# Kernel tuning notes

Hardware: AMD Instinct MI355X
Metric: run time of the kernel (lower is better)

The kernel has to match this reference:

```python
import jax, jax.numpy as jnp
import numpy as np

N = 100000
E = 1600000
IN_C, HID_C, OUT_C = 128, 128, 47


def setup_inputs() -> dict:
    key = jax.random.key(0)
    ks = jax.random.split(key, 10)
    x = jax.random.normal(ks[0], (N, IN_C), dtype=jnp.float32)
    edge_index = jax.random.randint(ks[1], (2, E), 0, N, dtype=jnp.int64)
    edge_attr = jax.random.normal(ks[2], (E, 8), dtype=jnp.float32)
    # GCNConv weights (glorot-like scale) and biases
    W1 = jax.random.normal(ks[3], (IN_C, HID_C), dtype=jnp.float32) / np.sqrt(IN_C)
    b1 = jnp.zeros((HID_C,), dtype=jnp.float32)
    W2 = jax.random.normal(ks[4], (HID_C, HID_C), dtype=jnp.float32) / np.sqrt(HID_C)
    b2 = jnp.zeros((HID_C,), dtype=jnp.float32)
    W3 = jax.random.normal(ks[5], (HID_C, OUT_C), dtype=jnp.float32) / np.sqrt(HID_C)
    b3 = jnp.zeros((OUT_C,), dtype=jnp.float32)
    return {"x": x, "edge_index": edge_index, "edge_attr": edge_attr,
            "W1": W1, "b1": b1, "W2": W2, "b2": b2, "W3": W3, "b3": b3}


def _gcn_norm(edge_index, num_nodes):
    # GCNConv default: add self-loops, symmetric normalization D^-1/2 (A+I) D^-1/2
    row, col = edge_index[0], edge_index[1]
    deg = jax.ops.segment_sum(jnp.ones((edge_index.shape[1],), jnp.float32), row,
                              num_segments=num_nodes) + 1.0  # +1 for self-loop
    dis = jax.lax.rsqrt(deg)  # deg >= 1, always finite
    edge_norm = dis[row] * dis[col]   # [E]
    self_norm = dis * dis             # [N], self-loop weight
    return edge_norm, self_norm


def _gcn_conv(h, W, b, row, col, edge_norm, self_norm, num_nodes):
    h = h @ W                                  # linear transform first (PyG order)
    msg = edge_norm[:, None] * h[col]          # [E, C] gathered, normalized messages
    agg = jax.ops.segment_sum(msg, row, num_segments=num_nodes)
    return agg + self_norm[:, None] * h + b    # self-loop contribution + bias


def reference(x, edge_index, edge_attr, W1, b1, W2, b2, W3, b3):
    # edge_attr is accepted but unused, matching the original forward.
    row, col = edge_index[0], edge_index[1]
    edge_norm, self_norm = _gcn_norm(edge_index, N)
    # layer 1 + relu (dropout is identity in eval mode)
    h = _gcn_conv(x, W1, b1, row, col, edge_norm, self_norm, N)
    h = jax.nn.relu(h)
    # layer 2 + relu
    h = _gcn_conv(h, W2, b2, row, col, edge_norm, self_norm, N)
    h = jax.nn.relu(h)
    # final layer, no activation
    return _gcn_conv(h, W3, b3, row, col, edge_norm, self_norm, N)
```

## Files before the change

### kernel.cpp

```cpp
#include <hip/hip_runtime.h>
#include <hip/hip_fp16.h>
#include <cstdint>
#include <cstddef>

#define N_NODES 100000
#define N_EDGES 1600000
#define BSHIFT 9
#define BSIZE (1 << BSHIFT)
#define NB ((N_NODES + BSIZE - 1) >> BSHIFT)
#define PTILE 4096

typedef _Float16 half8 __attribute__((ext_vector_type(8)));
typedef float floatx4 __attribute__((ext_vector_type(4)));
typedef int v4i __attribute__((ext_vector_type(4)));

__device__ float llvm_amdgcn_raw_buffer_load_fp32(v4i srsrc, int voffset,
                                                  int soffset, int aux)
    __asm("llvm.amdgcn.raw.buffer.load.f32");

static __device__ __forceinline__ v4i make_srsrc(const void* p) {
    unsigned long long a = (unsigned long long)p;
    v4i r;
    r[0] = (int)(unsigned)(a & 0xFFFFFFFFull);
    r[1] = (int)(unsigned)((a >> 32) & 0xFFFFull);
    r[2] = -1;
    r[3] = 0x00020000;
    return r;
}

static __device__ __forceinline__ __half2 f_as_h2(float f) {
    union { float f; __half2 h; } u; u.f = f; return u.h;
}

static __device__ __forceinline__ int edge_row(const void* ei, int i64, int e) {
    return i64 ? (int)((const long long*)ei)[e] : ((const int*)ei)[e];
}
static __device__ __forceinline__ int edge_col(const void* ei, int i64, int e) {
    return i64 ? (int)((const long long*)ei)[N_EDGES + e] : ((const int*)ei)[N_EDGES + e];
}

__global__ void __launch_bounds__(1024)
detect_i64(const int* __restrict__ w, int* __restrict__ flag,
           int* __restrict__ bsize) {
    __shared__ int red[1024];
    const int tid = threadIdx.x;
    if (tid < NB + 1) bsize[tid] = 0;
    int acc = 0;
    for (int j = tid; j < 2048; j += 1024) {
        int k = j * 781;
        acc |= w[2 * k + 1];
    }
    red[tid] = acc;
    __syncthreads();
    for (int off = 512; off > 0; off >>= 1) {
        if (tid < off) red[tid] |= red[tid + off];
        __syncthreads();
    }
    if (tid == 0) *flag = (red[0] == 0) ? 1 : 0;
}

__global__ void __launch_bounds__(256)
hist_buckets(const void* __restrict__ ei, const int* __restrict__ flag,
             int* __restrict__ bsize) {
    __shared__ int h[256];
    const int tid = threadIdx.x;
    const int tbase = blockIdx.x * PTILE;
    const int f = *flag;
    h[tid] = 0;
    __syncthreads();
    #pragma unroll
    for (int j = 0; j < PTILE / 256; ++j) {
        int idx = tbase + tid + j * 256;
        if (idx < N_EDGES) {
            int r = edge_row(ei, f, idx);
            atomicAdd(&h[r >> BSHIFT], 1);
        }
    }
    __syncthreads();
    if (tid < NB && h[tid] > 0) atomicAdd(&bsize[tid], h[tid]);
}

__global__ void scan_buckets(const int* __restrict__ bsize, int* __restrict__ bbase,
                             int* __restrict__ bcur) {
    __shared__ int sd[256];
    int t = threadIdx.x;
    int v = (t < NB) ? bsize[t] : 0;
    sd[t] = v;
    __syncthreads();
    for (int off = 1; off < 256; off <<= 1) {
        int add = (t >= off) ? sd[t - off] : 0;
        __syncthreads();
        sd[t] += add;
        __syncthreads();
    }
    if (t < NB) {
        bbase[t] = sd[t] - v;
        bcur[t] = sd[t] - v;
    }
    if (t == 255) bbase[NB] = sd[255];
}

__global__ void __launch_bounds__(256)
partition_edges(const void* __restrict__ ei, const int* __restrict__ flag,
                int* __restrict__ bcur, int* __restrict__ bktRow,
                int* __restrict__ bktCol) {
    __shared__ int rows[PTILE];
    __shared__ int cols[PTILE];
    __shared__ int h[256], sc[256], exs[256], base_s[256], p[256];

    const int tid = threadIdx.x;
    const int tbase = blockIdx.x * PTILE;
    const int tot = min(PTILE, N_EDGES - tbase);
    const int f = *flag;

    h[tid] = 0;
    p[tid] = 0;
    __syncthreads();

    #pragma unroll
    for (int j = 0; j < PTILE / 256; ++j) {
        int idx = tbase + tid + j * 256;
        if (idx < N_EDGES) {
            int r = edge_row(ei, f, idx);
            atomicAdd(&h[r >> BSHIFT], 1);
        }
    }
    __syncthreads();

    sc[tid] = h[tid];
    __syncthreads();
    for (int off = 1; off < 256; off <<= 1) {
        int v = (tid >= off) ? sc[tid - off] : 0;
        __syncthreads();
        sc[tid] += v;
        __syncthreads();
    }
    exs[tid] = sc[tid] - h[tid];
    if (tid < NB && h[tid] > 0) base_s[tid] = atomicAdd(&bcur[tid], h[tid]);
    __syncthreads();

    #pragma unroll
    for (int j = 0; j < PTILE / 256; ++j) {
        int idx = tbase + tid + j * 256;
        if (idx < N_EDGES) {
            int r = edge_row(ei, f, idx);
            int c = edge_col(ei, f, idx);
            int b = r >> BSHIFT;
            int lp = atomicAdd(&p[b], 1);
            int slot = exs[b] + lp;
            rows[slot] = r;
            cols[slot] = c;
        }
    }
    __syncthreads();

    for (int slot = tid; slot < tot; slot += 256) {
        int r = rows[slot];
        int b = r >> BSHIFT;
        int addr = base_s[b] + (slot - exs[b]);
        bktRow[addr] = r;
        bktCol[addr] = cols[slot];
    }
}

__global__ void __launch_bounds__(512)
bucket_stats(const int* __restrict__ bktRow, const int* __restrict__ bbase,
             int* __restrict__ deg, int* __restrict__ rowst,
             float* __restrict__ dis) {
    __shared__ int cnt[512];
    __shared__ int sd[512];
    const int b = blockIdx.x;
    const int t = threadIdx.x;
    const int start = bbase[b], end = bbase[b + 1];
    cnt[t] = 0;
    __syncthreads();
    for (int i = start + t; i < end; i += 512)
        atomicAdd(&cnt[bktRow[i] - (b << BSHIFT)], 1);
    __syncthreads();
    int v = cnt[t];
    sd[t] = v;
    __syncthreads();
    for (int off = 1; off < 512; off <<= 1) {
        int add = (t >= off) ? sd[t - off] : 0;
        __syncthreads();
        sd[t] += add;
        __syncthreads();
    }
    int node = (b << BSHIFT) + t;
    if (node < N_NODES) {
        deg[node] = v;
        rowst[node] = start + sd[t] - v;
        dis[node] = rsqrtf((float)v + 1.0f);
    }
}

__global__ void __launch_bounds__(512)
scatter_bucket(const int* __restrict__ bktRow, const int* __restrict__ bktCol,
               const int* __restrict__ bbase, const int* __restrict__ rowst,
               const float* __restrict__ dis, int2* __restrict__ csr_cn) {
    __shared__ int cur[512];
    __shared__ float dl[512];
    const int b = blockIdx.x;
    const int t = threadIdx.x;
    const int start = bbase[b], end = bbase[b + 1];
    int node = (b << BSHIFT) + t;
    cur[t] = (node < N_NODES) ? rowst[node] : 0;
    dl[t]  = (node < N_NODES) ? dis[node] : 0.f;
    __syncthreads();
    for (int i = start + t; i < end; i += 512) {
        int r = bktRow[i];
        int c = bktCol[i];
        int lr = r - (b << BSHIFT);
        int pos = atomicAdd(&cur[lr], 1);
        float nrm = dl[lr] * dis[c];
        csr_cn[pos] = make_int2(c, __float_as_int(nrm));
    }
}

template<typename TIn, int NT>
__global__ void __launch_bounds__(256)
gemm_mfma(const TIn* __restrict__ in, const float* __restrict__ W,
          __half* __restrict__ out, int Mfull, int ostride) {
    constexpr int NCOL = NT * 16;
    __shared__ _Float16 Wt[NCOL * 128];

    const int tid = threadIdx.x;
    for (int chunkIdx = tid; chunkIdx < NCOL * 16; chunkIdx += 256) {
        int n = chunkIdx % NCOL;
        int c = chunkIdx / NCOL;
        half8 v;
        #pragma unroll
        for (int i = 0; i < 8; ++i) {
            int k = c * 8 + i;
            v[i] = (n < Mfull) ? (_Float16)W[k * Mfull + n] : (_Float16)0.f;
        }
        *(half8*)&Wt[n * 128 + (c ^ (n & 7)) * 8] = v;
    }
    __syncthreads();

    const int wave = tid >> 6, lane = tid & 63;
    const int quad = lane >> 4, m = lane & 15;
    const int rowbase = blockIdx.x * 64 + wave * 16;
    const int arow_i = rowbase + m;
    const bool avalid = arow_i < N_NODES;
    const TIn* arow = in + (size_t)(avalid ? arow_i : 0) * 128;

    half8 a[4];
    #pragma unroll
    for (int kt = 0; kt < 4; ++kt) {
        if constexpr (sizeof(TIn) == 4) {
            const float4* ptr = (const float4*)((const float*)arow + kt * 32 + quad * 8);
            float4 f0 = ptr[0];
            float4 f1 = ptr[1];
            a[kt][0] = (_Float16)f0.x; a[kt][1] = (_Float16)f0.y;
            a[kt][2] = (_Float16)f0.z; a[kt][3] = (_Float16)f0.w;
            a[kt][4] = (_Float16)f1.x; a[kt][5] = (_Float16)f1.y;
            a[kt][6] = (_Float16)f1.z; a[kt][7] = (_Float16)f1.w;
        } else {
            a[kt] = *(const half8*)((const _Float16*)arow + kt * 32 + quad * 8);
        }
    }

    floatx4 acc[NT];
    #pragma unroll
    for (int ct = 0; ct < NT; ++ct) acc[ct] = (floatx4){0.f, 0.f, 0.f, 0.f};

    #pragma unroll
    for (int ct = 0; ct < NT; ++ct) {
        #pragma unroll
        for (int kt = 0; kt < 4; ++kt) {
            int n = ct * 16 + m;
            half8 bfrag = *(const half8*)&Wt[n * 128 + ((kt * 4 + quad) ^ (m & 7)) * 8];
            acc[ct] = __builtin_amdgcn_mfma_f32_16x16x32_f16(a[kt], bfrag, acc[ct], 0, 0, 0);
        }
    }

    const int rs0 = rowbase + quad * 4;
    #pragma unroll
    for (int ct = 0; ct < NT; ++ct) {
        int col = ct * 16 + m;
        if (col >= Mfull) continue;
        #pragma unroll
        for (int r = 0; r < 4; ++r) {
            int rs = rs0 + r;
            if (rs < N_NODES)
                out[(size_t)rs * ostride + col] = __float2half(acc[ct][r]);
        }
    }
}

#define AGG_DEPTH 6
#define AGG_BLOCKS 2048

__global__ void __launch_bounds__(256)
agg_c128(const __half* __restrict__ t, const int* __restrict__ rowst,
         const int* __restrict__ deg, const int2* __restrict__ cn,
         const float* __restrict__ dis, const float* __restrict__ bias,
         __half* __restrict__ out, int relu) {
    const int gwave = blockIdx.x * (blockDim.x >> 6) + (threadIdx.x >> 6);
    const int nw = gridDim.x * (blockDim.x >> 6);
    const int lane = threadIdx.x & 63;
    const float2 bv = ((const float2*)bias)[lane];
    const v4i trsrc = make_srsrc(t);
    const int voff_lane = lane << 2;

    for (int w = gwave; w < N_NODES; w += nw) {
        int s = rowst[w], d = deg[w];
        float di = dis[w];
        float sn = di * di;
        float2 tv = __half22float2(((const __half2*)(t + (size_t)w * 128))[lane]);
        float ax = fmaf(sn, tv.x, bv.x);
        float ay = fmaf(sn, tv.y, bv.y);
        int e = s + d;
        int j = s;
        if (j + AGG_DEPTH <= e) {
            int2 c[AGG_DEPTH];
            #pragma unroll
            for (int q = 0; q < AGG_DEPTH; ++q) c[q] = cn[j + q];
            j += AGG_DEPTH;
            while (j + AGG_DEPTH <= e) {
                int2 n[AGG_DEPTH];
                #pragma unroll
                for (int q = 0; q < AGG_DEPTH; ++q) n[q] = cn[j + q];
                __half2 v[AGG_DEPTH];
                #pragma unroll
                for (int q = 0; q < AGG_DEPTH; ++q)
                    v[q] = f_as_h2(llvm_amdgcn_raw_buffer_load_fp32(
                        trsrc, (c[q].x << 8) | voff_lane, 0, 1));
                #pragma unroll
                for (int q = 0; q < AGG_DEPTH; ++q) {
                    float2 fv = __half22float2(v[q]);
                    float nw2 = __int_as_float(c[q].y);
                    ax = fmaf(nw2, fv.x, ax);
                    ay = fmaf(nw2, fv.y, ay);
                }
                #pragma unroll
                for (int q = 0; q < AGG_DEPTH; ++q) c[q] = n[q];
                j += AGG_DEPTH;
            }
            #pragma unroll
            for (int q = 0; q < AGG_DEPTH; ++q) {
                __half2 vv = f_as_h2(llvm_amdgcn_raw_buffer_load_fp32(
                    trsrc, (c[q].x << 8) | voff_lane, 0, 1));
                float2 fv = __half22float2(vv);
                float nw2 = __int_as_float(c[q].y);
                ax = fmaf(nw2, fv.x, ax);
                ay = fmaf(nw2, fv.y, ay);
            }
        }
        for (; j < e; ++j) {
            int2 c = cn[j];
            __half2 vv = f_as_h2(llvm_amdgcn_raw_buffer_load_fp32(
                trsrc, (c.x << 8) | voff_lane, 0, 1));
            float2 fv = __half22float2(vv);
            float nw2 = __int_as_float(c.y);
            ax = fmaf(nw2, fv.x, ax);
            ay = fmaf(nw2, fv.y, ay);
        }
        if (relu) { ax = fmaxf(ax, 0.f); ay = fmaxf(ay, 0.f); }
        ((__half2*)(out + (size_t)w * 128))[lane] = __float22half2_rn(make_float2(ax, ay));
    }
}

#define C47_DEPTH 4

__global__ void __launch_bounds__(256)
agg_c47(const __half* __restrict__ t, const int* __restrict__ rowst,
        const int* __restrict__ deg, const int2* __restrict__ cn,
        const float* __restrict__ dis, const float* __restrict__ bias,
        float* __restrict__ out) {
    const int gwave = blockIdx.x * (blockDim.x >> 6) + (threadIdx.x >> 6);
    const int nw = gridDim.x * (blockDim.x >> 6);
    const int lane = threadIdx.x & 63;
    const int hw = lane >> 5;
    const int l2 = lane & 31;
    const int ch0 = l2 * 2, ch1 = ch0 + 1;
    const float b0 = (ch0 < 47) ? bias[ch0] : 0.f;
    const float b1 = (ch1 < 47) ? bias[ch1] : 0.f;

    for (int w = gwave; w < N_NODES; w += nw) {
        int s = rowst[w], d = deg[w];
        float di = dis[w];
        float sn = di * di;
        float2 tv = __half22float2(((const __half2*)(t + (size_t)w * 64))[l2]);
        float ax = (hw == 0) ? sn * tv.x : 0.f;
        float ay = (hw == 0) ? sn * tv.y : 0.f;
        int e = s + d;
        int j = s + hw;
        if (j + 2 * C47_DEPTH <= e + 1) {
            int2 c[C47_DEPTH];
            #pragma unroll
            for (int q = 0; q < C47_DEPTH; ++q) c[q] = cn[j + 2 * q];
            j += 2 * C47_DEPTH;
            while (j + 2 * C47_DEPTH <= e + 1) {
                int2 n[C47_DEPTH];
                #pragma unroll
                for (int q = 0; q < C47_DEPTH; ++q) n[q] = cn[j + 2 * q];
                __half2 v[C47_DEPTH];
                #pragma unroll
                for (int q = 0; q < C47_DEPTH; ++q)
                    v[q] = ((const __half2*)(t + (size_t)c[q].x * 64))[l2];
                #pragma unroll
                for (int q = 0; q < C47_DEPTH; ++q) {
                    float2 fv = __half22float2(v[q]);
                    float nw2 = __int_as_float(c[q].y);
                    ax = fmaf(nw2, fv.x, ax);
                    ay = fmaf(nw2, fv.y, ay);
                }
                #pragma unroll
                for (int q = 0; q < C47_DEPTH; ++q) c[q] = n[q];
                j += 2 * C47_DEPTH;
            }
            #pragma unroll
            for (int q = 0; q < C47_DEPTH; ++q) {
                __half2 vv = ((const __half2*)(t + (size_t)c[q].x * 64))[l2];
                float2 fv = __half22float2(vv);
                float nw2 = __int_as_float(c[q].y);
                ax = fmaf(nw2, fv.x, ax);
                ay = fmaf(nw2, fv.y, ay);
            }
        }
        for (; j < e; j += 2) {
            int2 c = cn[j];
            float2 fv = __half22float2(((const __half2*)(t + (size_t)c.x * 64))[l2]);
            float nw2 = __int_as_float(c.y);
            ax = fmaf(nw2, fv.x, ax);
            ay = fmaf(nw2, fv.y, ay);
        }
        ax += __shfl_xor(ax, 32);
        ay += __shfl_xor(ay, 32);
        if (hw == 0) {
            if (ch0 < 47) out[(size_t)w * 47 + ch0] = ax + b0;
            if (ch1 < 47) out[(size_t)w * 47 + ch1] = ay + b1;
        }
    }
}

extern "C" void kernel_launch(void* const* d_in, const int* in_sizes, int n_in,
                              void* d_out, int out_size, void* d_ws, size_t ws_size,
                              hipStream_t stream) {
    const float* x  = (const float*)d_in[0];
    const void*  ei = d_in[1];
    const float* W1 = (const float*)d_in[3];
    const float* b1 = (const float*)d_in[4];
    const float* W2 = (const float*)d_in[5];
    const float* b2 = (const float*)d_in[6];
    const float* W3 = (const float*)d_in[7];
    const float* b3 = (const float*)d_in[8];
    float* out = (float*)d_out;

    size_t off = 0;
    auto alloc = [&](size_t bytes) -> void* {
        void* p = (char*)d_ws + off;
        off += (bytes + 511) & ~(size_t)511;
        return p;
    };
    float*  dis     = (float*)alloc((size_t)N_NODES * 4);
    int*    deg     = (int*)  alloc((size_t)N_NODES * 4);
    int*    rowst   = (int*)  alloc((size_t)N_NODES * 4);
    int*    bsize   = (int*)  alloc((NB + 1) * 4);
    int*    bbase   = (int*)  alloc((NB + 1) * 4);
    int*    bcur    = (int*)  alloc(NB * 4);
    int*    flag    = (int*)  alloc(64);
    int2*   csr_cn  = (int2*) alloc((size_t)N_EDGES * 8);
    __half* tbuf    = (__half*)alloc((size_t)N_NODES * 128 * 2);
    __half* hbuf    = (__half*)alloc((size_t)N_NODES * 128 * 2);
    int*    bktRow  = (int*)hbuf;
    int*    bktCol  = bktRow + N_EDGES;
    (void)ws_size; (void)in_sizes; (void)n_in; (void)out_size;

    int ptiles = (N_EDGES + PTILE - 1) / PTILE;

    detect_i64<<<1, 1024, 0, stream>>>((const int*)ei, flag, bsize);
    hist_buckets<<<ptiles, 256, 0, stream>>>(ei, flag, bsize);
    scan_buckets<<<1, 256, 0, stream>>>(bsize, bbase, bcur);
    partition_edges<<<ptiles, 256, 0, stream>>>(ei, flag, bcur, bktRow, bktCol);
    bucket_stats<<<NB, 512, 0, stream>>>(bktRow, bbase, deg, rowst, dis);
    scatter_bucket<<<NB, 512, 0, stream>>>(bktRow, bktCol, bbase, rowst, dis, csr_cn);

    int gblocks = (N_NODES + 63) / 64;

    gemm_mfma<float, 8><<<gblocks, 256, 0, stream>>>(x, W1, tbuf, 128, 128);
    agg_c128<<<AGG_BLOCKS, 256, 0, stream>>>(tbuf, rowst, deg, csr_cn, dis, b1, hbuf, 1);
    gemm_mfma<_Float16, 8><<<gblocks, 256, 0, stream>>>((_Float16*)hbuf, W2, tbuf, 128, 128);
    agg_c128<<<AGG_BLOCKS, 256, 0, stream>>>(tbuf, rowst, deg, csr_cn, dis, b2, hbuf, 1);
    gemm_mfma<_Float16, 3><<<gblocks, 256, 0, stream>>>((_Float16*)hbuf, W3, tbuf, 47, 64);
    agg_c47<<<AGG_BLOCKS, 256, 0, stream>>>(tbuf, rowst, deg, csr_cn, dis, b3, out);
}
```

Baseline: 495.3 us.

## Store hidden features in 16-channel slices and aggregate per slice

The 128-channel hidden features are now stored as eight column slices of 16 half values per node. The GEMM kernels read and write this sliced layout, and a new aggregation kernel gives each block one slice. Each wave splits across 8 edges at a time and reduces with shuffles. The aim is to keep each slice's gather working set (3.2MB) small enough for cache, improving locality of the random neighbour gathers. The cost is 32-byte gathers per edge, 8x re-reading of the CSR edge list, and the loss of the deep buffer-load pipelining.

```diff
diff --git a/kernel.cpp b/kernel.cpp
--- a/kernel.cpp
+++ b/kernel.cpp
@@ -10,27 +10,11 @@
 #define NB ((N_NODES + BSIZE - 1) >> BSHIFT)
 #define PTILE 4096
 
+#define NSLICE 8
+#define SLICE_STRIDE ((size_t)N_NODES * 16)
+
 typedef _Float16 half8 __attribute__((ext_vector_type(8)));
 typedef float floatx4 __attribute__((ext_vector_type(4)));
-typedef int v4i __attribute__((ext_vector_type(4)));
-
-__device__ float llvm_amdgcn_raw_buffer_load_fp32(v4i srsrc, int voffset,
-                                                  int soffset, int aux)
-    __asm("llvm.amdgcn.raw.buffer.load.f32");
-
-static __device__ __forceinline__ v4i make_srsrc(const void* p) {
-    unsigned long long a = (unsigned long long)p;
-    v4i r;
-    r[0] = (int)(unsigned)(a & 0xFFFFFFFFull);
-    r[1] = (int)(unsigned)((a >> 32) & 0xFFFFull);
-    r[2] = -1;
-    r[3] = 0x00020000;
-    return r;
-}
-
-static __device__ __forceinline__ __half2 f_as_h2(float f) {
-    union { float f; __half2 h; } u; u.f = f; return u.h;
-}
 
 static __device__ __forceinline__ int edge_row(const void* ei, int i64, int e) {
     return i64 ? (int)((const long long*)ei)[e] : ((const int*)ei)[e];
@@ -217,7 +201,7 @@
     }
 }
 
-template<typename TIn, int NT>
+template<typename TIn, int NT, bool SIN, bool SOUT>
 __global__ void __launch_bounds__(256)
 gemm_mfma(const TIn* __restrict__ in, const float* __restrict__ W,
           __half* __restrict__ out, int Mfull, int ostride) {
@@ -242,14 +226,19 @@
     const int quad = lane >> 4, m = lane & 15;
     const int rowbase = blockIdx.x * 64 + wave * 16;
     const int arow_i = rowbase + m;
-    const bool avalid = arow_i < N_NODES;
-    const TIn* arow = in + (size_t)(avalid ? arow_i : 0) * 128;
+    const int arow_cl = (arow_i < N_NODES) ? arow_i : 0;
 
     half8 a[4];
     #pragma unroll
     for (int kt = 0; kt < 4; ++kt) {
-        if constexpr (sizeof(TIn) == 4) {
-            const float4* ptr = (const float4*)((const float*)arow + kt * 32 + quad * 8);
+        if constexpr (SIN) {
+            int sc = kt * 2 + (quad >> 1);
+            const _Float16* src = (const _Float16*)in
+                + (size_t)sc * SLICE_STRIDE + (size_t)arow_cl * 16 + (quad & 1) * 8;
+            a[kt] = *(const half8*)src;
+        } else if constexpr (sizeof(TIn) == 4) {
+            const float* arow = (const float*)in + (size_t)arow_cl * 128;
+            const float4* ptr = (const float4*)(arow + kt * 32 + quad * 8);
             float4 f0 = ptr[0];
             float4 f1 = ptr[1];
             a[kt][0] = (_Float16)f0.x; a[kt][1] = (_Float16)f0.y;
@@ -257,7 +246,8 @@
             a[kt][4] = (_Float16)f1.x; a[kt][5] = (_Float16)f1.y;
             a[kt][6] = (_Float16)f1.z; a[kt][7] = (_Float16)f1.w;
         } else {
-            a[kt] = *(const half8*)((const _Float16*)arow + kt * 32 + quad * 8);
+            const _Float16* arow = (const _Float16*)in + (size_t)arow_cl * 128;
+            a[kt] = *(const half8*)(arow + kt * 32 + quad * 8);
         }
     }
 
@@ -283,86 +273,67 @@
         #pragma unroll
         for (int r = 0; r < 4; ++r) {
             int rs = rs0 + r;
-            if (rs < N_NODES)
-                out[(size_t)rs * ostride + col] = __float2half(acc[ct][r]);
-        }
-    }
-}
-
-#define AGG_DEPTH 6
+            if (rs < N_NODES) {
+                if constexpr (SOUT)
+                    out[(size_t)ct * SLICE_STRIDE + (size_t)rs * 16 + m] =
+                        __float2half(acc[ct][r]);
+                else
+                    out[(size_t)rs * ostride + col] = __float2half(acc[ct][r]);
+            }
+        }
+    }
+}
+
+__global__ void __launch_bounds__(256)
+agg_c128_sl(const __half* __restrict__ ts, const int* __restrict__ rowst,
+            const int* __restrict__ deg, const int2* __restrict__ cn,
+            const float* __restrict__ dis, const float* __restrict__ bias,
+            __half* __restrict__ outs, int relu) {
+    const int slice = blockIdx.x & 7;
+    const int sblk  = blockIdx.x >> 3;
+    const int nsb   = gridDim.x >> 3;
+    const int wave  = threadIdx.x >> 6;
+    const int lane  = threadIdx.x & 63;
+    const int g     = lane >> 3;
+    const int p     = lane & 7;
+    const __half* tsl = ts + (size_t)slice * SLICE_STRIDE;
+    __half* osl = outs + (size_t)slice * SLICE_STRIDE;
+    const float2 bv = *(const float2*)(bias + slice * 16 + p * 2);
+
+    for (int w = sblk * 4 + wave; w < N_NODES; w += nsb * 4) {
+        int s = rowst[w], d = deg[w];
+        float di = dis[w], sn = di * di;
+        float ax = 0.f, ay = 0.f;
+        if (g == 0) {
+            float2 tv = __half22float2(*(const __half2*)(tsl + (size_t)w * 16 + p * 2));
+            ax = sn * tv.x; ay = sn * tv.y;
+        }
+        int e = s + d;
+        int rounds = (d + 7) >> 3;
+        int j = s + g;
+        for (int r = 0; r < rounds; ++r, j += 8) {
+            bool act = j < e;
+            int2 c = act ? cn[j] : make_int2(0, 0);
+            float2 fv = __half22float2(
+                *(const __half2*)(tsl + (size_t)c.x * 16 + p * 2));
+            float nw = __int_as_float(c.y);
+            ax = fmaf(nw, fv.x, ax);
+            ay = fmaf(nw, fv.y, ay);
+        }
+        ax += __shfl_xor(ax, 8);  ay += __shfl_xor(ay, 8);
+        ax += __shfl_xor(ax, 16); ay += __shfl_xor(ay, 16);
+        ax += __shfl_xor(ax, 32); ay += __shfl_xor(ay, 32);
+        if (g == 0) {
+            ax += bv.x; ay += bv.y;
+            if (relu) { ax = fmaxf(ax, 0.f); ay = fmaxf(ay, 0.f); }
+            *(__half2*)(osl + (size_t)w * 16 + p * 2) =
+                __float22half2_rn(make_float2(ax, ay));
+        }
+    }
+}
+
+#define C47_DEPTH 4
 #define AGG_BLOCKS 2048
-
-__global__ void __launch_bounds__(256)
-agg_c128(const __half* __restrict__ t, const int* __restrict__ rowst,
-         const int* __restrict__ deg, const int2* __restrict__ cn,
-         const float* __restrict__ dis, const float* __restrict__ bias,
-         __half* __restrict__ out, int relu) {
-    const int gwave = blockIdx.x * (blockDim.x >> 6) + (threadIdx.x >> 6);
-    const int nw = gridDim.x * (blockDim.x >> 6);
-    const int lane = threadIdx.x & 63;
-    const float2 bv = ((const float2*)bias)[lane];
-    const v4i trsrc = make_srsrc(t);
-    const int voff_lane = lane << 2;
-
-    for (int w = gwave; w < N_NODES; w += nw) {
-        int s = rowst[w], d = deg[w];
-        float di = dis[w];
-        float sn = di * di;
-        float2 tv = __half22float2(((const __half2*)(t + (size_t)w * 128))[lane]);
-        float ax = fmaf(sn, tv.x, bv.x);
-        float ay = fmaf(sn, tv.y, bv.y);
-        int e = s + d;
-        int j = s;
-        if (j + AGG_DEPTH <= e) {
-            int2 c[AGG_DEPTH];
-            #pragma unroll
-            for (int q = 0; q < AGG_DEPTH; ++q) c[q] = cn[j + q];
-            j += AGG_DEPTH;
-            while (j + AGG_DEPTH <= e) {
-                int2 n[AGG_DEPTH];
-                #pragma unroll
-                for (int q = 0; q < AGG_DEPTH; ++q) n[q] = cn[j + q];
-                __half2 v[AGG_DEPTH];
-                #pragma unroll
-                for (int q = 0; q < AGG_DEPTH; ++q)
-                    v[q] = f_as_h2(llvm_amdgcn_raw_buffer_load_fp32(
-                        trsrc, (c[q].x << 8) | voff_lane, 0, 1));
-                #pragma unroll
-                for (int q = 0; q < AGG_DEPTH; ++q) {
-                    float2 fv = __half22float2(v[q]);
-                    float nw2 = __int_as_float(c[q].y);
-                    ax = fmaf(nw2, fv.x, ax);
-                    ay = fmaf(nw2, fv.y, ay);
-                }
-                #pragma unroll
-                for (int q = 0; q < AGG_DEPTH; ++q) c[q] = n[q];
-                j += AGG_DEPTH;
-            }
-            #pragma unroll
-            for (int q = 0; q < AGG_DEPTH; ++q) {
-                __half2 vv = f_as_h2(llvm_amdgcn_raw_buffer_load_fp32(
-                    trsrc, (c[q].x << 8) | voff_lane, 0, 1));
-                float2 fv = __half22float2(vv);
-                float nw2 = __int_as_float(c[q].y);
-                ax = fmaf(nw2, fv.x, ax);
-                ay = fmaf(nw2, fv.y, ay);
-            }
-        }
-        for (; j < e; ++j) {
-            int2 c = cn[j];
-            __half2 vv = f_as_h2(llvm_amdgcn_raw_buffer_load_fp32(
-                trsrc, (c.x << 8) | voff_lane, 0, 1));
-            float2 fv = __half22float2(vv);
-            float nw2 = __int_as_float(c.y);
-            ax = fmaf(nw2, fv.x, ax);
-            ay = fmaf(nw2, fv.y, ay);
-        }
-        if (relu) { ax = fmaxf(ax, 0.f); ay = fmaxf(ay, 0.f); }
-        ((__half2*)(out + (size_t)w * 128))[lane] = __float22half2_rn(make_float2(ax, ay));
-    }
-}
-
-#define C47_DEPTH 4
 
 __global__ void __launch_bounds__(256)
 agg_c47(const __half* __restrict__ t, const int* __restrict__ rowst,
@@ -467,6 +438,7 @@
     __half* hbuf    = (__half*)alloc((size_t)N_NODES * 128 * 2);
     int*    bktRow  = (int*)hbuf;
     int*    bktCol  = bktRow + N_EDGES;
+    __half* t3      = tbuf;
     (void)ws_size; (void)in_sizes; (void)n_in; (void)out_size;
 
     int ptiles = (N_EDGES + PTILE - 1) / PTILE;
@@ -480,10 +452,12 @@
 
     int gblocks = (N_NODES + 63) / 64;
 
-    gemm_mfma<float, 8><<<gblocks, 256, 0, stream>>>(x, W1, tbuf, 128, 128);
-    agg_c128<<<AGG_BLOCKS, 256, 0, stream>>>(tbuf, rowst, deg, csr_cn, dis, b1, hbuf, 1);
-    gemm_mfma<_Float16, 8><<<gblocks, 256, 0, stream>>>((_Float16*)hbuf, W2, tbuf, 128, 128);
-    agg_c128<<<AGG_BLOCKS, 256, 0, stream>>>(tbuf, rowst, deg, csr_cn, dis, b2, hbuf, 1);
-    gemm_mfma<_Float16, 3><<<gblocks, 256, 0, stream>>>((_Float16*)hbuf, W3, tbuf, 47, 64);
-    agg_c47<<<AGG_BLOCKS, 256, 0, stream>>>(tbuf, rowst, deg, csr_cn, dis, b3, out);
-}
+    gemm_mfma<float, 8, false, true><<<gblocks, 256, 0, stream>>>(x, W1, tbuf, 128, 0);
+    agg_c128_sl<<<2048, 256, 0, stream>>>(tbuf, rowst, deg, csr_cn, dis, b1, hbuf, 1);
+    gemm_mfma<_Float16, 8, true, true><<<gblocks, 256, 0, stream>>>(
+        (_Float16*)hbuf, W2, tbuf, 128, 0);
+    agg_c128_sl<<<2048, 256, 0, stream>>>(tbuf, rowst, deg, csr_cn, dis, b2, hbuf, 1);
+    gemm_mfma<_Float16, 3, true, false><<<gblocks, 256, 0, stream>>>(
+        (_Float16*)hbuf, W3, t3, 47, 64);
+    agg_c47<<<AGG_BLOCKS, 256, 0, stream>>>(t3, rowst, deg, csr_cn, dis, b3, out);
+}
```

Result: slower. 773.0 us (+56.1%).

## Drop bucket histogram pass by using fixed-capacity edge buckets

Applied to the files above, without the earlier changes.

Removes the separate histogram kernel that reads all edge rows to size the buckets. Instead, each bucket gets a fixed slot range of BCAP entries, partition_edges appends into it with a per-bucket cursor, and the prefix scan runs afterwards on the final cursor counts to get CSR offsets. This saves one full read of the row indices and one kernel launch. The risk is that any bucket receiving more than BCAP edges overflows into the next bucket. That holds for uniformly random indices but not for skewed graphs.

```diff
diff --git a/kernel.cpp b/kernel.cpp
--- a/kernel.cpp
+++ b/kernel.cpp
@@ -9,6 +9,7 @@
 #define BSIZE (1 << BSHIFT)
 #define NB ((N_NODES + BSIZE - 1) >> BSHIFT)
 #define PTILE 4096
+#define BCAP 12288
 
 typedef _Float16 half8 __attribute__((ext_vector_type(8)));
 typedef float floatx4 __attribute__((ext_vector_type(4)));
@@ -41,10 +42,10 @@
 
 __global__ void __launch_bounds__(1024)
 detect_i64(const int* __restrict__ w, int* __restrict__ flag,
-           int* __restrict__ bsize) {
+           int* __restrict__ bcur) {
     __shared__ int red[1024];
     const int tid = threadIdx.x;
-    if (tid < NB + 1) bsize[tid] = 0;
+    if (tid < NB) bcur[tid] = tid * BCAP;
     int acc = 0;
     for (int j = tid; j < 2048; j += 1024) {
         int k = j * 781;
@@ -57,47 +58,6 @@
         __syncthreads();
     }
     if (tid == 0) *flag = (red[0] == 0) ? 1 : 0;
-}
-
-__global__ void __launch_bounds__(256)
-hist_buckets(const void* __restrict__ ei, const int* __restrict__ flag,
-             int* __restrict__ bsize) {
-    __shared__ int h[256];
-    const int tid = threadIdx.x;
-    const int tbase = blockIdx.x * PTILE;
-    const int f = *flag;
-    h[tid] = 0;
-    __syncthreads();
-    #pragma unroll
-    for (int j = 0; j < PTILE / 256; ++j) {
-        int idx = tbase + tid + j * 256;
-        if (idx < N_EDGES) {
-            int r = edge_row(ei, f, idx);
-            atomicAdd(&h[r >> BSHIFT], 1);
-        }
-    }
-    __syncthreads();
-    if (tid < NB && h[tid] > 0) atomicAdd(&bsize[tid], h[tid]);
-}
-
-__global__ void scan_buckets(const int* __restrict__ bsize, int* __restrict__ bbase,
-                             int* __restrict__ bcur) {
-    __shared__ int sd[256];
-    int t = threadIdx.x;
-    int v = (t < NB) ? bsize[t] : 0;
-    sd[t] = v;
-    __syncthreads();
-    for (int off = 1; off < 256; off <<= 1) {
-        int add = (t >= off) ? sd[t - off] : 0;
-        __syncthreads();
-        sd[t] += add;
-        __syncthreads();
-    }
-    if (t < NB) {
-        bbase[t] = sd[t] - v;
-        bcur[t] = sd[t] - v;
-    }
-    if (t == 255) bbase[NB] = sd[255];
 }
 
 __global__ void __launch_bounds__(256)
@@ -163,15 +123,31 @@
     }
 }
 
+__global__ void scan_buckets(const int* __restrict__ bcur, int* __restrict__ bbase) {
+    __shared__ int sd[256];
+    int t = threadIdx.x;
+    int v = (t < NB) ? (bcur[t] - t * BCAP) : 0;
+    sd[t] = v;
+    __syncthreads();
+    for (int off = 1; off < 256; off <<= 1) {
+        int add = (t >= off) ? sd[t - off] : 0;
+        __syncthreads();
+        sd[t] += add;
+        __syncthreads();
+    }
+    if (t < NB) bbase[t] = sd[t] - v;
+    if (t == 255) bbase[NB] = sd[255];
+}
+
 __global__ void __launch_bounds__(512)
-bucket_stats(const int* __restrict__ bktRow, const int* __restrict__ bbase,
-             int* __restrict__ deg, int* __restrict__ rowst,
-             float* __restrict__ dis) {
+bucket_stats(const int* __restrict__ bktRow, const int* __restrict__ bcur,
+             const int* __restrict__ bbase, int* __restrict__ deg,
+             int* __restrict__ rowst, float* __restrict__ dis) {
     __shared__ int cnt[512];
     __shared__ int sd[512];
     const int b = blockIdx.x;
     const int t = threadIdx.x;
-    const int start = bbase[b], end = bbase[b + 1];
+    const int start = b * BCAP, end = bcur[b];
     cnt[t] = 0;
     __syncthreads();
     for (int i = start + t; i < end; i += 512)
@@ -189,20 +165,20 @@
     int node = (b << BSHIFT) + t;
     if (node < N_NODES) {
         deg[node] = v;
-        rowst[node] = start + sd[t] - v;
+        rowst[node] = bbase[b] + sd[t] - v;
         dis[node] = rsqrtf((float)v + 1.0f);
     }
 }
 
 __global__ void __launch_bounds__(512)
 scatter_bucket(const int* __restrict__ bktRow, const int* __restrict__ bktCol,
-               const int* __restrict__ bbase, const int* __restrict__ rowst,
+               const int* __restrict__ bcur, const int* __restrict__ rowst,
                const float* __restrict__ dis, int2* __restrict__ csr_cn) {
     __shared__ int cur[512];
     __shared__ float dl[512];
     const int b = blockIdx.x;
     const int t = threadIdx.x;
-    const int start = bbase[b], end = bbase[b + 1];
+    const int start = b * BCAP, end = bcur[b];
     int node = (b << BSHIFT) + t;
     cur[t] = (node < N_NODES) ? rowst[node] : 0;
     dl[t]  = (node < N_NODES) ? dis[node] : 0.f;
@@ -458,7 +434,6 @@
     float*  dis     = (float*)alloc((size_t)N_NODES * 4);
     int*    deg     = (int*)  alloc((size_t)N_NODES * 4);
     int*    rowst   = (int*)  alloc((size_t)N_NODES * 4);
-    int*    bsize   = (int*)  alloc((NB + 1) * 4);
     int*    bbase   = (int*)  alloc((NB + 1) * 4);
     int*    bcur    = (int*)  alloc(NB * 4);
     int*    flag    = (int*)  alloc(64);
@@ -466,17 +441,16 @@
     __half* tbuf    = (__half*)alloc((size_t)N_NODES * 128 * 2);
     __half* hbuf    = (__half*)alloc((size_t)N_NODES * 128 * 2);
     int*    bktRow  = (int*)hbuf;
-    int*    bktCol  = bktRow + N_EDGES;
+    int*    bktCol  = bktRow + (size_t)NB * BCAP;
     (void)ws_size; (void)in_sizes; (void)n_in; (void)out_size;
 
     int ptiles = (N_EDGES + PTILE - 1) / PTILE;
 
-    detect_i64<<<1, 1024, 0, stream>>>((const int*)ei, flag, bsize);
-    hist_buckets<<<ptiles, 256, 0, stream>>>(ei, flag, bsize);
-    scan_buckets<<<1, 256, 0, stream>>>(bsize, bbase, bcur);
+    detect_i64<<<1, 1024, 0, stream>>>((const int*)ei, flag, bcur);
     partition_edges<<<ptiles, 256, 0, stream>>>(ei, flag, bcur, bktRow, bktCol);
-    bucket_stats<<<NB, 512, 0, stream>>>(bktRow, bbase, deg, rowst, dis);
-    scatter_bucket<<<NB, 512, 0, stream>>>(bktRow, bktCol, bbase, rowst, dis, csr_cn);
+    scan_buckets<<<1, 256, 0, stream>>>(bcur, bbase);
+    bucket_stats<<<NB, 512, 0, stream>>>(bktRow, bcur, bbase, deg, rowst, dis);
+    scatter_bucket<<<NB, 512, 0, stream>>>(bktRow, bktCol, bcur, rowst, dis, csr_cn);
 
     int gblocks = (N_NODES + 63) / 64;
 
```

After: 503.0 us. No clear change (+1.6%).
